# Performance work log

Hardware: AMD Instinct MI355X
Metric: run time of the kernel (lower is better)

Reference implementation:

```python
import jax, jax.numpy as jnp
import numpy as np

WINDOW = 7
NUM_HEADS = 16
HEAD_DIM = 32  # dim 512 / 16 heads
SCALE = HEAD_DIM ** -0.5


def _relative_position_index(ws: int) -> np.ndarray:
    coords = np.stack(np.meshgrid(np.arange(ws), np.arange(ws), indexing='ij'))  # [2, ws, ws]
    flat = coords.reshape(2, -1)  # [2, N]
    rel = flat[:, :, None] - flat[:, None, :]  # [2, N, N]
    rel = rel.transpose(1, 2, 0)  # [N, N, 2]
    rh = (rel[:, :, 0] + ws - 1) * (2 * ws - 1)
    rw = rel[:, :, 1] + ws - 1
    return (rh + rw).astype(np.int32)  # [N, N]

REL_IDX = jnp.asarray(_relative_position_index(WINDOW))  # [49, 49]


def setup_inputs() -> dict:
    key = jax.random.key(0)
    ks = jax.random.split(key, 4)
    B, N, C = 4096, WINDOW * WINDOW, 512
    x = jax.random.normal(ks[0], (B, N, C), dtype=jnp.float32)
    qkv_w = jax.random.normal(ks[1], (C, 3 * C), dtype=jnp.float32) * (C ** -0.5)
    qkv_b = jnp.zeros((3 * C,), dtype=jnp.float32)
    proj_w = jax.random.normal(ks[2], (C, C), dtype=jnp.float32) * (C ** -0.5)
    proj_b = jnp.zeros((C,), dtype=jnp.float32)
    bias_table = jax.random.normal(ks[3], ((2 * WINDOW - 1) ** 2, NUM_HEADS), dtype=jnp.float32) * 0.02
    return {"x": x, "qkv_w": qkv_w, "qkv_b": qkv_b, "proj_w": proj_w,
            "proj_b": proj_b, "bias_table": bias_table}


def reference(x, qkv_w, qkv_b, proj_w, proj_b, bias_table):
    B, N, C = x.shape
    # QKV projection -> [B, N, 3, H, D] -> q/k/v [B, H, N, D]
    qkv = (x @ qkv_w + qkv_b).reshape(B, N, 3, NUM_HEADS, HEAD_DIM)
    qkv = jnp.transpose(qkv, (2, 0, 3, 1, 4))
    q, k, v = qkv[0], qkv[1], qkv[2]
    attn = jnp.einsum('bhnd,bhmd->bhnm', q * SCALE, k)  # [B, H, N, N]
    # relative position bias gather: [N*N, H] -> [1, H, N, N]
    bias = bias_table[REL_IDX.reshape(-1)].reshape(N, N, NUM_HEADS)
    attn = attn + jnp.transpose(bias, (2, 0, 1))[None]
    attn = jax.nn.softmax(attn, axis=-1)
    out = jnp.einsum('bhnm,bhmd->bhnd', attn, v)  # [B, H, N, D]
    out = jnp.transpose(out, (0, 2, 1, 3)).reshape(B, N, C)
    return out @ proj_w + proj_b
```

## Files before the change

### kernel.cpp

```cpp
#include <hip/hip_runtime.h>

typedef _Float16 h16;
typedef __attribute__((ext_vector_type(4))) _Float16 h16x4;
typedef __attribute__((ext_vector_type(8))) _Float16 h16x8;
typedef __attribute__((ext_vector_type(4))) float f32x4;

#define QSCALE 0.25505653882616254f
#define LOG2E  1.4426950408889634f
#define MFMA16(a, b, c) __builtin_amdgcn_mfma_f32_16x16x16f16(a, b, c, 0, 0, 0)
#define MFMA32(a, b, c) __builtin_amdgcn_mfma_f32_16x16x32_f16(a, b, c, 0, 0, 0)

#define O_BYTES 205520896ULL
#define W1F_OFF (O_BYTES)
#define W2T_OFF (W1F_OFF + 1572864ULL)
#define BF_OFF  (W2T_OFF + 524288ULL)

__global__ __launch_bounds__(256) void wa_prep(
    const float* __restrict__ qkv_w, const float* __restrict__ proj_w,
    const float* __restrict__ table,
    h16* __restrict__ w1F, h16* __restrict__ w2T, float* __restrict__ biasF) {
  __shared__ h16 T[32][33];
  const int b = blockIdx.x, tid = threadIdx.x;
  if (b < 256) {
    int tx = tid & 31, ty = tid >> 5;
    int bo = b & 15, bc = b >> 4;
    #pragma unroll
    for (int i = 0; i < 4; ++i) {
      int c = bc * 32 + ty + 8 * i, o = bo * 32 + tx;
      T[ty + 8 * i][tx] = (h16)proj_w[c * 512 + o];
    }
    __syncthreads();
    #pragma unroll
    for (int i = 0; i < 4; ++i) {
      int o_l = ty + 8 * i;
      w2T[(size_t)(bo * 32 + o_l) * 512 + bc * 32 + tx] = T[tx][o_l];
    }
  } else if (b < 640) {
    int chunk = (b - 256) * 256 + tid;
    int lane = chunk & 63;
    int rest = chunk >> 6;
    int f  = rest % 12;
    int kt = (rest / 12) & 7;
    int wv = (rest / 96) & 3;
    int g  = rest / 384;
    int s = f >> 2, d = (f >> 1) & 1, ks = f & 1;
    int l15 = lane & 15, lg = lane >> 4;
    int o = s * 512 + g * 128 + wv * 32 + d * 16 + l15;
    int k0 = kt * 64 + ks * 32 + lg * 8;
    float sc = (s == 0) ? QSCALE : 1.0f;
    h16x8 v;
    #pragma unroll
    for (int e = 0; e < 8; ++e)
      v[e] = (h16)(qkv_w[(size_t)(k0 + e) * 1536 + o] * sc);
    *(h16x8*)(w1F + (size_t)chunk * 8) = v;
  } else {
    int t = (b - 640) * 256 + tid;
    int lane = t & 63, jt = (t >> 6) & 3, qt = (t >> 8) & 3, head = t >> 10;
    int l15 = lane & 15, lg = lane >> 4;
    int q = qt * 16 + l15;
    float4 v;
    #pragma unroll
    for (int r = 0; r < 4; ++r) {
      int j = jt * 16 + lg * 4 + r;
      float val = -1e30f;
      if (j < 49 && q < 49) {
        int rel = (q / 7 - j / 7 + 6) * 13 + (q % 7 - j % 7 + 6);
        val = table[rel * 16 + head] * LOG2E;
      }
      ((float*)&v)[r] = val;
    }
    ((float4*)biasF)[t] = v;
  }
}

__global__ __launch_bounds__(256, 2) void wa_qkv_attn(
    const float* __restrict__ x, const float* __restrict__ qkv_b,
    const h16* __restrict__ w1F, const float* __restrict__ biasF,
    h16* __restrict__ O) {
  __shared__ __align__(16) char lds[50176];
  const int tid = threadIdx.x;
  const int wave = tid >> 6, lane = tid & 63;
  const int l15 = lane & 15, lg = lane >> 4;
  const int sw = l15 & 7;
  const int lbid = (blockIdx.x & 7) * 1024 + (blockIdx.x >> 3);
  const int w = lbid >> 1, gp = lbid & 1;
  const size_t rowbase = (size_t)w * 49;

  #pragma unroll
  for (int p = 0; p < 13; ++p) {
    int idx = tid + p * 256;
    if (idx < 3136) {
      int r = idx >> 6, c = idx & 63;
      const float* src = x + (rowbase + r) * 512 + c * 8;
      float4 a = *(const float4*)(src);
      float4 bb = *(const float4*)(src + 4);
      h16x8 h = { (h16)a.x, (h16)a.y, (h16)a.z, (h16)a.w,
                  (h16)bb.x, (h16)bb.y, (h16)bb.z, (h16)bb.w };
      *(h16x8*)(lds + r * 1024 + ((c ^ (r & 7)) << 4)) = h;
    }
  }
  __syncthreads();

  int xb[4], coA[4], coB[4];
  #pragma unroll
  for (int t = 0; t < 4; ++t) {
    int row = (t < 3) ? (16 * t + l15) : 48;
    int swt = (t < 3) ? sw : 0;
    xb[t] = row * 1024;
    coA[t] = ((lg ^ swt) << 4);
    coB[t] = (((4 + lg) ^ swt) << 4);
  }
  const h16x4 ones = (h16x4){(h16)1.f, (h16)1.f, (h16)1.f, (h16)1.f};
  const float4* bF4 = (const float4*)biasF;

#define WLOAD(DST, KT) {                                                   \
    _Pragma("unroll") for (int f = 0; f < 12; ++f)                         \
      DST[f] = *(const h16x8*)(wb + (size_t)(KT) * 6144 + f * 512); }

#define GSTEP(KT, W) {                                                     \
    h16x8 xf[4];                                                           \
    _Pragma("unroll") for (int t = 0; t < 4; ++t)                          \
      xf[t] = *(const h16x8*)(lds + xb[t] + coA[t] + (KT) * 128);          \
    __builtin_amdgcn_s_setprio(1);                                         \
    _Pragma("unroll") for (int d = 0; d < 2; ++d)                          \
    _Pragma("unroll") for (int t = 0; t < 4; ++t) {                        \
      accQ[d][t] = MFMA32(W[0 + d*2], xf[t], accQ[d][t]);                  \
      accK[d][t] = MFMA32(W[4 + d*2], xf[t], accK[d][t]);                  \
      accV[t][d] = MFMA32(xf[t], W[8 + d*2], accV[t][d]);                  \
    }                                                                      \
    __builtin_amdgcn_s_setprio(0);                                         \
    _Pragma("unroll") for (int t = 0; t < 4; ++t)                          \
      xf[t] = *(const h16x8*)(lds + xb[t] + coB[t] + (KT) * 128);          \
    __builtin_amdgcn_s_setprio(1);                                         \
    _Pragma("unroll") for (int d = 0; d < 2; ++d)                          \
    _Pragma("unroll") for (int t = 0; t < 4; ++t) {                        \
      accQ[d][t] = MFMA32(W[1 + d*2], xf[t], accQ[d][t]);                  \
      accK[d][t] = MFMA32(W[5 + d*2], xf[t], accK[d][t]);                  \
      accV[t][d] = MFMA32(xf[t], W[9 + d*2], accV[t][d]);                  \
    }                                                                      \
    __builtin_amdgcn_s_setprio(0); }

#define PROCESS_HEAD(G) {                                                  \
    const int head = (G) * 4 + wave;                                       \
    const h16* wb = w1F + ((size_t)((G) * 4 + wave) * 8) * 6144 + lane * 8;\
    f32x4 accQ[2][4], accK[2][4], accV[4][2];                              \
    _Pragma("unroll") for (int d = 0; d < 2; ++d)                          \
    _Pragma("unroll") for (int t = 0; t < 4; ++t) {                        \
      accQ[d][t] = (f32x4){0.f, 0.f, 0.f, 0.f};                            \
      accK[d][t] = (f32x4){0.f, 0.f, 0.f, 0.f};                            \
      accV[t][d] = (f32x4){0.f, 0.f, 0.f, 0.f};                            \
    }                                                                      \
    h16x8 WA[12], WB[12];                                                  \
    WLOAD(WA, 0);                                                          \
    for (int kt2 = 0; kt2 < 4; ++kt2) {                                    \
      WLOAD(WB, 2 * kt2 + 1);                                              \
      GSTEP(2 * kt2, WA);                                                  \
      if (kt2 < 3) WLOAD(WA, 2 * kt2 + 2);                                 \
      GSTEP(2 * kt2 + 1, WB);                                              \
    }                                                                      \
    float bq[2][4], bk[2][4], bv[2];                                       \
    _Pragma("unroll") for (int d = 0; d < 2; ++d) {                        \
      _Pragma("unroll") for (int r = 0; r < 4; ++r) {                      \
        bq[d][r] = qkv_b[head * 32 + 16 * d + 4 * lg + r] * QSCALE;        \
        bk[d][r] = qkv_b[512 + head * 32 + 16 * d + 4 * lg + r];           \
      }                                                                    \
      bv[d] = qkv_b[1024 + head * 32 + 16 * d + l15];                      \
    }                                                                      \
    h16x4 Qh[2][4], Kh[2][4], Vh[4][2];                                    \
    _Pragma("unroll") for (int d = 0; d < 2; ++d)                          \
    _Pragma("unroll") for (int t = 0; t < 4; ++t)                          \
    _Pragma("unroll") for (int r = 0; r < 4; ++r) {                        \
      Qh[d][t][r] = (h16)(accQ[d][t][r] + bq[d][r]);                       \
      Kh[d][t][r] = (h16)(accK[d][t][r] + bk[d][r]);                       \
      Vh[t][d][r] = (h16)(accV[t][d][r] + bv[d]);                          \
    }                                                                      \
             \
    f32x4 st[4][4];                                                        \
    __builtin_amdgcn_s_setprio(1);                                         \
    _Pragma("unroll") for (int jt = 0; jt < 4; ++jt)                       \
    _Pragma("unroll") for (int qt = 0; qt < 4; ++qt) {                     \
      float4 bvv = bF4[(head * 16 + qt * 4 + jt) * 64 + lane];             \
      f32x4 c0 = { bvv.x, bvv.y, bvv.z, bvv.w };                           \
      st[jt][qt] = MFMA16(Kh[0][jt], Qh[0][qt], c0);                       \
      st[jt][qt] = MFMA16(Kh[1][jt], Qh[1][qt], st[jt][qt]);               \
    }                                                                      \
    __builtin_amdgcn_s_setprio(0);                                         \
    h16x4 pf[4][4];                                                        \
    _Pragma("unroll") for (int qt = 0; qt < 4; ++qt)                       \
    _Pragma("unroll") for (int jt = 0; jt < 4; ++jt) {                     \
      h16x4 p;                                                             \
      _Pragma("unroll") for (int r = 0; r < 4; ++r)                        \
        p[r] = (h16)exp2f(st[jt][qt][r]);                                  \
      pf[jt][qt] = p;                                                      \
    }                                                                      \
    f32x4 ss[4];                                                           \
    _Pragma("unroll") for (int qt = 0; qt < 4; ++qt)                       \
      ss[qt] = (f32x4){0.f, 0.f, 0.f, 0.f};                                \
    f32x4 ot[2][4];                                                        \
    _Pragma("unroll") for (int d = 0; d < 2; ++d)                          \
    _Pragma("unroll") for (int qt = 0; qt < 4; ++qt)                       \
      ot[d][qt] = (f32x4){0.f, 0.f, 0.f, 0.f};                             \
    __builtin_amdgcn_s_setprio(1);                                         \
    _Pragma("unroll") for (int jt = 0; jt < 4; ++jt)                       \
    _Pragma("unroll") for (int qt = 0; qt < 4; ++qt) {                     \
      ss[qt] = MFMA16(ones, pf[jt][qt], ss[qt]);                           \
      _Pragma("unroll") for (int d = 0; d < 2; ++d)                        \
        ot[d][qt] = MFMA16(Vh[jt][d], pf[jt][qt], ot[d][qt]);              \
    }                                                                      \
    __builtin_amdgcn_s_setprio(0);                                         \
    _Pragma("unroll") for (int qt = 0; qt < 4; ++qt) {                     \
      int q = 16 * qt + l15;                                               \
      float ri = 1.0f / ss[qt][0];                                         \
      if (q < 49) {                                                        \
        h16* gdst = O + (rowbase + q) * 512 + head * 32 + 4 * lg;          \
        _Pragma("unroll") for (int d = 0; d < 2; ++d) {                    \
          h16x4 ov;                                                        \
          _Pragma("unroll") for (int r = 0; r < 4; ++r)                    \
            ov[r] = (h16)(ot[d][qt][r] * ri);                              \
          *(h16x4*)(gdst + 16 * d) = ov;                                   \
        }                                                                  \
      }                                                                    \
    } }

  PROCESS_HEAD(gp * 2);
  PROCESS_HEAD(gp * 2 + 1);
#undef PROCESS_HEAD
#undef WLOAD
#undef GSTEP
}

__global__ __launch_bounds__(256, 3) void wa_proj(
    const h16* __restrict__ O, const h16* __restrict__ w2T,
    const float* __restrict__ proj_b, float* __restrict__ out) {
  __shared__ __align__(16) char lds[32768];
  char* Ac = lds;
  char* Bc = lds + 16384;
  const int tid = threadIdx.x;
  const int wave = tid >> 6, lane = tid & 63;
  const int l15 = lane & 15, lg = lane >> 4;
  const int lbid = (blockIdx.x & 7) * 784 + (blockIdx.x >> 3);
  const int rowt = lbid >> 2, colt = lbid & 3;
  const int wr = wave >> 1, wc = wave & 1;

  f32x4 acc[4][4];
  #pragma unroll
  for (int a = 0; a < 4; ++a)
    #pragma unroll
    for (int b = 0; b < 4; ++b) acc[a][b] = (f32x4){0.f, 0.f, 0.f, 0.f};

  h16x8 pre[8];
  #pragma unroll
  for (int p = 0; p < 8; ++p) {
    int idx = tid + p * 256;
    int r = (idx >> 3) & 127, c = idx & 7;
    pre[p] = (idx < 1024)
        ? *(const h16x8*)(O   + (size_t)(rowt * 128 + r) * 512 + c * 8)
        : *(const h16x8*)(w2T + (size_t)(colt * 128 + r) * 512 + c * 8);
  }
  #pragma unroll
  for (int p = 0; p < 8; ++p) {
    int idx = tid + p * 256;
    int r = (idx >> 3) & 127, c = idx & 7;
    char* dst = ((idx < 1024) ? Ac : Bc) + r * 128 + ((c ^ (r & 7)) << 4);
    *(h16x8*)dst = pre[p];
  }
  __syncthreads();

  for (int kt = 0; kt < 8; ++kt) {
    if (kt < 7) {
      #pragma unroll
      for (int p = 0; p < 8; ++p) {
        int idx = tid + p * 256;
        int r = (idx >> 3) & 127, c = idx & 7;
        pre[p] = (idx < 1024)
            ? *(const h16x8*)(O   + (size_t)(rowt * 128 + r) * 512 + (kt + 1) * 64 + c * 8)
            : *(const h16x8*)(w2T + (size_t)(colt * 128 + r) * 512 + (kt + 1) * 64 + c * 8);
      }
    }
    #pragma unroll
    for (int kh = 0; kh < 2; ++kh) {
      const int cc = kh * 4 + lg;
      const int sw = (l15 & 7);
      h16x8 af[4], bf[4];
      #pragma unroll
      for (int mt = 0; mt < 4; ++mt) {
        int r = wr * 64 + 16 * mt + l15;
        af[mt] = *(const h16x8*)(Ac + r * 128 + ((cc ^ sw) << 4));
      }
      #pragma unroll
      for (int nt = 0; nt < 4; ++nt) {
        int r = wc * 64 + 16 * nt + l15;
        bf[nt] = *(const h16x8*)(Bc + r * 128 + ((cc ^ sw) << 4));
      }
      __builtin_amdgcn_s_setprio(1);
      #pragma unroll
      for (int mt = 0; mt < 4; ++mt)
        #pragma unroll
        for (int nt = 0; nt < 4; ++nt)
          acc[mt][nt] = MFMA32(af[mt], bf[nt], acc[mt][nt]);
      __builtin_amdgcn_s_setprio(0);
    }
    __syncthreads();
    if (kt < 7) {
      #pragma unroll
      for (int p = 0; p < 8; ++p) {
        int idx = tid + p * 256;
        int r = (idx >> 3) & 127, c = idx & 7;
        char* dst = ((idx < 1024) ? Ac : Bc) + r * 128 + ((c ^ (r & 7)) << 4);
        *(h16x8*)dst = pre[p];
      }
      __syncthreads();
    }
  }
  #pragma unroll
  for (int nt = 0; nt < 4; ++nt) {
    int col = colt * 128 + wc * 64 + nt * 16 + l15;
    float pb = proj_b[col];
    #pragma unroll
    for (int mt = 0; mt < 4; ++mt) {
      int row = rowt * 128 + wr * 64 + mt * 16 + 4 * lg;
      #pragma unroll
      for (int r = 0; r < 4; ++r)
        out[(size_t)(row + r) * 512 + col] = acc[mt][nt][r] + pb;
    }
  }
}

extern "C" void kernel_launch(void* const* d_in, const int* in_sizes, int n_in,
                              void* d_out, int out_size, void* d_ws, size_t ws_size,
                              hipStream_t stream) {
  const float* x          = (const float*)d_in[0];
  const float* qkv_w      = (const float*)d_in[1];
  const float* qkv_b      = (const float*)d_in[2];
  const float* proj_w     = (const float*)d_in[3];
  const float* proj_b     = (const float*)d_in[4];
  const float* bias_table = (const float*)d_in[5];
  float* out = (float*)d_out;

  char* ws = (char*)d_ws;
  h16*   O     = (h16*)ws;
  h16*   w1F   = (h16*)(ws + W1F_OFF);
  h16*   w2T   = (h16*)(ws + W2T_OFF);
  float* biasF = (float*)(ws + BF_OFF);

  wa_prep<<<704, 256, 0, stream>>>(qkv_w, proj_w, bias_table, w1F, w2T, biasF);
  wa_qkv_attn<<<8192, 256, 0, stream>>>(x, qkv_b, w1F, biasF, O);
  wa_proj<<<1568 * 4, 256, 0, stream>>>(O, w2T, proj_b, out);
}
```

Baseline: 701.4 us.

## Split fused QKV GEMM into separate Q, K, V passes to cut registers

The fused per-head QKV projection, which held 24 accumulators and 24 weight fragments live at once, becomes three sequential passes (Q, K, V). Each pass keeps only 8 accumulators and 8 weight fragments, and the launch bound rises from 2 to 3 blocks per CU to use the lower register pressure for occupancy. The cost is that the x tile is read from LDS three times instead of once per k-step, and the MFMA chains between loads are shorter, so latency hiding within a wave gets worse. LDS use of about 49 KB per block may also limit the third block per CU.

```diff
diff --git a/kernel.cpp b/kernel.cpp
--- a/kernel.cpp
+++ b/kernel.cpp
@@ -73,7 +73,7 @@
   }
 }
 
-__global__ __launch_bounds__(256, 2) void wa_qkv_attn(
+__global__ __launch_bounds__(256, 3) void wa_qkv_attn(
     const float* __restrict__ x, const float* __restrict__ qkv_b,
     const h16* __restrict__ w1F, const float* __restrict__ biasF,
     h16* __restrict__ O) {
@@ -101,80 +101,113 @@
   }
   __syncthreads();
 
-  int xb[4], coA[4], coB[4];
+  int xbA[4], xbB[4];
   #pragma unroll
   for (int t = 0; t < 4; ++t) {
     int row = (t < 3) ? (16 * t + l15) : 48;
     int swt = (t < 3) ? sw : 0;
-    xb[t] = row * 1024;
-    coA[t] = ((lg ^ swt) << 4);
-    coB[t] = (((4 + lg) ^ swt) << 4);
+    xbA[t] = row * 1024 + ((lg ^ swt) << 4);
+    xbB[t] = row * 1024 + (((4 + lg) ^ swt) << 4);
   }
   const h16x4 ones = (h16x4){(h16)1.f, (h16)1.f, (h16)1.f, (h16)1.f};
   const float4* bF4 = (const float4*)biasF;
 
-#define WLOAD(DST, KT) {                                                   \
-    _Pragma("unroll") for (int f = 0; f < 12; ++f)                         \
-      DST[f] = *(const h16x8*)(wb + (size_t)(KT) * 6144 + f * 512); }
-
-#define GSTEP(KT, W) {                                                     \
+#define WLOAD4(DST, S, KT) {                                               \
+    _Pragma("unroll") for (int f4 = 0; f4 < 4; ++f4)                       \
+      DST[f4] = *(const h16x8*)(wb + (size_t)(KT) * 6144 + ((S)*4 + f4) * 512); }
+
+#define STEP_WA(KT, W, ACC) {                                              \
     h16x8 xf[4];                                                           \
     _Pragma("unroll") for (int t = 0; t < 4; ++t)                          \
-      xf[t] = *(const h16x8*)(lds + xb[t] + coA[t] + (KT) * 128);          \
-    __builtin_amdgcn_s_setprio(1);                                         \
-    _Pragma("unroll") for (int d = 0; d < 2; ++d)                          \
-    _Pragma("unroll") for (int t = 0; t < 4; ++t) {                        \
-      accQ[d][t] = MFMA32(W[0 + d*2], xf[t], accQ[d][t]);                  \
-      accK[d][t] = MFMA32(W[4 + d*2], xf[t], accK[d][t]);                  \
-      accV[t][d] = MFMA32(xf[t], W[8 + d*2], accV[t][d]);                  \
-    }                                                                      \
+      xf[t] = *(const h16x8*)(lds + xbA[t] + (KT) * 128);                  \
+    __builtin_amdgcn_s_setprio(1);                                         \
+    _Pragma("unroll") for (int d = 0; d < 2; ++d)                          \
+    _Pragma("unroll") for (int t = 0; t < 4; ++t)                          \
+      ACC[d][t] = MFMA32(W[d*2], xf[t], ACC[d][t]);                        \
     __builtin_amdgcn_s_setprio(0);                                         \
     _Pragma("unroll") for (int t = 0; t < 4; ++t)                          \
-      xf[t] = *(const h16x8*)(lds + xb[t] + coB[t] + (KT) * 128);          \
-    __builtin_amdgcn_s_setprio(1);                                         \
-    _Pragma("unroll") for (int d = 0; d < 2; ++d)                          \
-    _Pragma("unroll") for (int t = 0; t < 4; ++t) {                        \
-      accQ[d][t] = MFMA32(W[1 + d*2], xf[t], accQ[d][t]);                  \
-      accK[d][t] = MFMA32(W[5 + d*2], xf[t], accK[d][t]);                  \
-      accV[t][d] = MFMA32(xf[t], W[9 + d*2], accV[t][d]);                  \
-    }                                                                      \
+      xf[t] = *(const h16x8*)(lds + xbB[t] + (KT) * 128);                  \
+    __builtin_amdgcn_s_setprio(1);                                         \
+    _Pragma("unroll") for (int d = 0; d < 2; ++d)                          \
+    _Pragma("unroll") for (int t = 0; t < 4; ++t)                          \
+      ACC[d][t] = MFMA32(W[d*2 + 1], xf[t], ACC[d][t]);                    \
     __builtin_amdgcn_s_setprio(0); }
+
+#define STEP_XA(KT, W, ACC) {                                              \
+    h16x8 xf[4];                                                           \
+    _Pragma("unroll") for (int t = 0; t < 4; ++t)                          \
+      xf[t] = *(const h16x8*)(lds + xbA[t] + (KT) * 128);                  \
+    __builtin_amdgcn_s_setprio(1);                                         \
+    _Pragma("unroll") for (int d = 0; d < 2; ++d)                          \
+    _Pragma("unroll") for (int t = 0; t < 4; ++t)                          \
+      ACC[t][d] = MFMA32(xf[t], W[d*2], ACC[t][d]);                        \
+    __builtin_amdgcn_s_setprio(0);                                         \
+    _Pragma("unroll") for (int t = 0; t < 4; ++t)                          \
+      xf[t] = *(const h16x8*)(lds + xbB[t] + (KT) * 128);                  \
+    __builtin_amdgcn_s_setprio(1);                                         \
+    _Pragma("unroll") for (int d = 0; d < 2; ++d)                          \
+    _Pragma("unroll") for (int t = 0; t < 4; ++t)                          \
+      ACC[t][d] = MFMA32(xf[t], W[d*2 + 1], ACC[t][d]);                    \
+    __builtin_amdgcn_s_setprio(0); }
+
+#define GPASS(S, STEP, ACC) {                                              \
+    h16x8 Wa[4], Wb[4];                                                    \
+    WLOAD4(Wa, S, 0);                                                      \
+    for (int kt2 = 0; kt2 < 4; ++kt2) {                                    \
+      WLOAD4(Wb, S, 2 * kt2 + 1);                                          \
+      STEP(2 * kt2, Wa, ACC);                                              \
+      if (kt2 < 3) WLOAD4(Wa, S, 2 * kt2 + 2);                             \
+      STEP(2 * kt2 + 1, Wb, ACC);                                          \
+    } }
 
 #define PROCESS_HEAD(G) {                                                  \
     const int head = (G) * 4 + wave;                                       \
     const h16* wb = w1F + ((size_t)((G) * 4 + wave) * 8) * 6144 + lane * 8;\
-    f32x4 accQ[2][4], accK[2][4], accV[4][2];                              \
-    _Pragma("unroll") for (int d = 0; d < 2; ++d)                          \
-    _Pragma("unroll") for (int t = 0; t < 4; ++t) {                        \
-      accQ[d][t] = (f32x4){0.f, 0.f, 0.f, 0.f};                            \
-      accK[d][t] = (f32x4){0.f, 0.f, 0.f, 0.f};                            \
-      accV[t][d] = (f32x4){0.f, 0.f, 0.f, 0.f};                            \
-    }                                                                      \
-    h16x8 WA[12], WB[12];                                                  \
-    WLOAD(WA, 0);                                                          \
-    for (int kt2 = 0; kt2 < 4; ++kt2) {                                    \
-      WLOAD(WB, 2 * kt2 + 1);                                              \
-      GSTEP(2 * kt2, WA);                                                  \
-      if (kt2 < 3) WLOAD(WA, 2 * kt2 + 2);                                 \
-      GSTEP(2 * kt2 + 1, WB);                                              \
-    }                                                                      \
-    float bq[2][4], bk[2][4], bv[2];                                       \
-    _Pragma("unroll") for (int d = 0; d < 2; ++d) {                        \
-      _Pragma("unroll") for (int r = 0; r < 4; ++r) {                      \
-        bq[d][r] = qkv_b[head * 32 + 16 * d + 4 * lg + r] * QSCALE;        \
-        bk[d][r] = qkv_b[512 + head * 32 + 16 * d + 4 * lg + r];           \
+    h16x4 Qh[2][4], Kh[2][4], Vh[4][2];                                    \
+     {                                               \
+      f32x4 acc[2][4];                                                     \
+      _Pragma("unroll") for (int d = 0; d < 2; ++d)                        \
+      _Pragma("unroll") for (int t = 0; t < 4; ++t)                        \
+        acc[d][t] = (f32x4){0.f, 0.f, 0.f, 0.f};                           \
+      GPASS(0, STEP_WA, acc);                                              \
+      _Pragma("unroll") for (int d = 0; d < 2; ++d) {                      \
+        float bq[4];                                                       \
+        _Pragma("unroll") for (int r = 0; r < 4; ++r)                      \
+          bq[r] = qkv_b[head * 32 + 16 * d + 4 * lg + r] * QSCALE;         \
+        _Pragma("unroll") for (int t = 0; t < 4; ++t)                      \
+        _Pragma("unroll") for (int r = 0; r < 4; ++r)                      \
+          Qh[d][t][r] = (h16)(acc[d][t][r] + bq[r]);                       \
       }                                                                    \
-      bv[d] = qkv_b[1024 + head * 32 + 16 * d + l15];                      \
-    }                                                                      \
-    h16x4 Qh[2][4], Kh[2][4], Vh[4][2];                                    \
-    _Pragma("unroll") for (int d = 0; d < 2; ++d)                          \
-    _Pragma("unroll") for (int t = 0; t < 4; ++t)                          \
-    _Pragma("unroll") for (int r = 0; r < 4; ++r) {                        \
-      Qh[d][t][r] = (h16)(accQ[d][t][r] + bq[d][r]);                       \
-      Kh[d][t][r] = (h16)(accK[d][t][r] + bk[d][r]);                       \
-      Vh[t][d][r] = (h16)(accV[t][d][r] + bv[d]);                          \
-    }                                                                      \
-             \
+    }                                                                      \
+     {                                               \
+      f32x4 acc[2][4];                                                     \
+      _Pragma("unroll") for (int d = 0; d < 2; ++d)                        \
+      _Pragma("unroll") for (int t = 0; t < 4; ++t)                        \
+        acc[d][t] = (f32x4){0.f, 0.f, 0.f, 0.f};                           \
+      GPASS(1, STEP_WA, acc);                                              \
+      _Pragma("unroll") for (int d = 0; d < 2; ++d) {                      \
+        float bk[4];                                                       \
+        _Pragma("unroll") for (int r = 0; r < 4; ++r)                      \
+          bk[r] = qkv_b[512 + head * 32 + 16 * d + 4 * lg + r];            \
+        _Pragma("unroll") for (int t = 0; t < 4; ++t)                      \
+        _Pragma("unroll") for (int r = 0; r < 4; ++r)                      \
+          Kh[d][t][r] = (h16)(acc[d][t][r] + bk[r]);                       \
+      }                                                                    \
+    }                                                                      \
+     {                                               \
+      f32x4 acc[4][2];                                                     \
+      _Pragma("unroll") for (int t = 0; t < 4; ++t)                        \
+      _Pragma("unroll") for (int d = 0; d < 2; ++d)                        \
+        acc[t][d] = (f32x4){0.f, 0.f, 0.f, 0.f};                           \
+      GPASS(2, STEP_XA, acc);                                              \
+      _Pragma("unroll") for (int d = 0; d < 2; ++d) {                      \
+        float bv = qkv_b[1024 + head * 32 + 16 * d + l15];                 \
+        _Pragma("unroll") for (int t = 0; t < 4; ++t)                      \
+        _Pragma("unroll") for (int r = 0; r < 4; ++r)                      \
+          Vh[t][d][r] = (h16)(acc[t][d][r] + bv);                          \
+      }                                                                    \
+    }                                                                      \
+                             \
     f32x4 st[4][4];                                                        \
     __builtin_amdgcn_s_setprio(1);                                         \
     _Pragma("unroll") for (int jt = 0; jt < 4; ++jt)                       \
@@ -225,8 +258,10 @@
   PROCESS_HEAD(gp * 2);
   PROCESS_HEAD(gp * 2 + 1);
 #undef PROCESS_HEAD
-#undef WLOAD
-#undef GSTEP
+#undef GPASS
+#undef STEP_WA
+#undef STEP_XA
+#undef WLOAD4
 }
 
 __global__ __launch_bounds__(256, 3) void wa_proj(
```

Result: no change. 696.9 us (-0.6%).
